# Kernel tuning notes

Measured on AMD Instinct MI355X. Metric: run time of the kernel, lower is better.

Reference implementation:

```python
import jax, jax.numpy as jnp
import numpy as np
from jax.scipy.special import logsumexp

# Model config: alphabet='ACGTZY', collapse='ACGTCA' -> 4 canonical bases, 2 mods
NBASE = 4
NTRANS = 2 * NBASE * (NBASE + 1)          # 40 flip-flop transition states
CAN_NMODS = np.array([1, 1, 0, 0])        # mods per canonical base (A:Y, C:Z)
SIZE = NTRANS + 1 + int(CAN_NMODS.sum())  # 43 linear outputs
LARGE_LOG_VAL = np.float32(50000.0)
T, N, INSIZE = 2000, 128, 256


def _can_indices():
    """Per-canonical-base index groups into the mod block of the linear output."""
    idx, cur = [], 0
    for nm in CAN_NMODS:
        idx.append(np.concatenate([[0], np.arange(cur + 1, cur + 1 + nm)]))
        cur += nm
    return idx

CAN_INDICES = _can_indices()


def setup_inputs() -> dict:
    key = jax.random.key(0)
    k1, k2, k3 = jax.random.split(key, 3)
    x = jax.random.normal(k1, (T, N, INSIZE), dtype=jnp.float32)
    W = jax.random.normal(k2, (SIZE, INSIZE), dtype=jnp.float32) / np.float32(INSIZE ** 0.5)
    b = jax.random.normal(k3, (SIZE,), dtype=jnp.float32) * 0.1
    return {"x": x, "W": W, "b": b}


def global_norm_flipflop(scores):
    """Log-partition of the flip-flop CRF via a sequential log-space scan.

    scores: (T, N, 2*nbase*(nbase+1)).
    """
    Tn, Nn, _ = scores.shape
    # initial state: flip states uniform, flop states ~ -inf
    fwd0 = jnp.concatenate(
        [jnp.zeros((Nn, NBASE), scores.dtype),
         jnp.full((Nn, NBASE), -LARGE_LOG_VAL, scores.dtype)], axis=1)
    logZ0 = logsumexp(fwd0, axis=1, keepdims=True)
    fwd0 = fwd0 - logZ0

    def step(carry, scores_t):
        fwd, logZ = carry
        # (N, nbase+1, 2*nbase): dest-state x source-state transition scores
        curr = fwd[:, None, :] + scores_t.reshape(Nn, NBASE + 1, 2 * NBASE)
        base1 = logsumexp(curr[:, :NBASE], axis=2)                    # to-flip states
        base2 = jnp.logaddexp(curr[:, NBASE, :NBASE],
                              curr[:, NBASE, NBASE:])                 # to-flop (stay)
        new = jnp.concatenate([base1, base2], axis=1)                 # (N, 2*nbase)
        fac = logsumexp(new, axis=1, keepdims=True)
        return (new - fac, logZ + fac), None

    (_, logZ), _ = jax.lax.scan(step, (fwd0, logZ0), scores)
    return scores - logZ / np.float32(Tn)


def reference(x, W, b):
    # Linear projection: (T, N, insize) -> (T, N, size)
    y = jnp.einsum('tnf,cf->tnc', x, W) + b
    # Globally-normalized flip-flop transition scores
    trans = global_norm_flipflop(y[:, :, :NTRANS])
    # Per-canonical-base categorical (can + its mods) log-softmax scores
    mods = [jax.nn.log_softmax(y[:, :, NTRANS + idx], axis=2) for idx in CAN_INDICES]
    return jnp.concatenate([trans] + mods, axis=2)
```

## Files before the change

kernel.cpp:

```cpp
#include <hip/hip_runtime.h>

#define T_DIM 2000
#define N_DIM 128
#define IN_DIM 256
#define OUT_C 46
#define NROWS (T_DIM * N_DIM)
#define NCHUNK 250
#define CLEN 8
#define NSUPER 25
#define SLEN 10

typedef short bf16x8 __attribute__((ext_vector_type(8)));
typedef float f32x4 __attribute__((ext_vector_type(4)));

union F8U { bf16x8 v; uint32_t u[4]; };

__device__ __forceinline__ uint32_t cvtpk(float lo, float hi) {
  uint32_t r;
  asm("v_cvt_pk_bf16_f32 %0, %1, %2" : "=v"(r) : "v"(lo), "v"(hi));
  return r;
}

__device__ __forceinline__ float bf2f(unsigned short u) {
  uint32_t w = (uint32_t)u << 16;
  return __builtin_bit_cast(float, w);
}

#define LDSK 264

__global__ __launch_bounds__(512, 2) void k1_gemm(const float* __restrict__ x,
                                                  const float* __restrict__ W,
                                                  const float* __restrict__ b,
                                                  unsigned short* __restrict__ wsYT,
                                                  float* __restrict__ wsMod) {
  __shared__ unsigned short Wl[43 * LDSK];
  const int tid  = threadIdx.x;
  const int lane = tid & 63;
  const int wv   = tid >> 6;
  const int ln   = lane & 15;
  const int lh   = lane >> 4;

  {
    uint32_t* Wd = reinterpret_cast<uint32_t*>(Wl);
#pragma unroll
    for (int it = 0; it < 11; ++it) {
      int e = tid + it * 512;
      if (e < 43 * 128) {
        int n = e >> 7, kp = e & 127;
        float2 w = *reinterpret_cast<const float2*>(W + (size_t)n * IN_DIM + 2 * kp);
        Wd[n * (LDSK / 2) + kp] = cvtpk(w.x, w.y);
      }
    }
  }
  float bias[3];
#pragma unroll
  for (int nt = 0; nt < 3; ++nt) {
    int n = nt * 16 + ln;
    bias[nt] = b[n > 42 ? 42 : n];
  }
  __syncthreads();

  const int rowbase = blockIdx.x * 512 + wv * 64;
  const float* xbase = x + (size_t)(rowbase + ln) * IN_DIM + lh * 8;

  f32x4 bufA[8], bufB[8];
  f32x4 zero = {0.f, 0.f, 0.f, 0.f};
  f32x4 acc[3] = {zero, zero, zero};

#define LOADH(BUF, T, HF) do {                                               \
    const float* _p = xbase + (size_t)(T) * (16 * IN_DIM) + (HF) * 128;      \
    _Pragma("unroll")                                                        \
    for (int _s = 0; _s < 4; ++_s) {                                         \
      BUF[_s]     = *reinterpret_cast<const f32x4*>(_p + _s * 32);           \
      BUF[_s + 4] = *reinterpret_cast<const f32x4*>(_p + _s * 32 + 4);       \
    }                                                                        \
  } while (0)

#define COMPH(BUF, HF) do {                                                  \
    _Pragma("unroll")                                                        \
    for (int _s2 = 0; _s2 < 4; ++_s2) {                                      \
      F8U _af;                                                               \
      _af.u[0] = cvtpk(BUF[_s2].x, BUF[_s2].y);                              \
      _af.u[1] = cvtpk(BUF[_s2].z, BUF[_s2].w);                              \
      _af.u[2] = cvtpk(BUF[_s2 + 4].x, BUF[_s2 + 4].y);                      \
      _af.u[3] = cvtpk(BUF[_s2 + 4].z, BUF[_s2 + 4].w);                      \
      const int _s = (HF) * 4 + _s2;                                         \
      _Pragma("unroll")                                                      \
      for (int _nt = 0; _nt < 3; ++_nt) {                                    \
        const bf16x8 _bf = *reinterpret_cast<const bf16x8*>(                 \
            &Wl[(_nt * 16 + ln) * LDSK + _s * 32 + lh * 8]);                 \
        acc[_nt] = __builtin_amdgcn_mfma_f32_16x16x32_bf16(_af.v, _bf,       \
                                                           acc[_nt], 0, 0, 0);\
      }                                                                      \
    }                                                                        \
  } while (0)

  LOADH(bufA, 0, 0);
  LOADH(bufB, 0, 1);
#pragma unroll 1
  for (int t = 0; t < 4; ++t) {
    COMPH(bufA, 0);
    if (t < 3) LOADH(bufA, t + 1, 0);
    COMPH(bufB, 1);
    if (t < 3) LOADH(bufB, t + 1, 1);
    const int R0 = rowbase + t * 16;
    const int tt = R0 >> 7;
    const int n0 = (R0 & 127) + lh * 4;
#pragma unroll
    for (int nt = 0; nt < 3; ++nt) {
      const int c = nt * 16 + ln;
      if (nt < 2 || ln < 8) {
        uint32_t d0 = cvtpk(acc[nt][0] + bias[nt], acc[nt][1] + bias[nt]);
        uint32_t d1 = cvtpk(acc[nt][2] + bias[nt], acc[nt][3] + bias[nt]);
        uint2 v; v.x = d0; v.y = d1;
        *reinterpret_cast<uint2*>(wsYT + ((size_t)tt * 40 + c) * 128 + n0) = v;
      } else if (ln < 11) {
        float4 v;
        v.x = acc[2][0] + bias[2]; v.y = acc[2][1] + bias[2];
        v.z = acc[2][2] + bias[2]; v.w = acc[2][3] + bias[2];
        *reinterpret_cast<float4*>(
            wsMod + ((size_t)tt * 3 + (ln - 8)) * 128 + n0) = v;
      }
      acc[nt] = zero;
    }
  }
#undef LOADH
#undef COMPH
}

__global__ __launch_bounds__(128, 1) void k2a_chunk(const unsigned short* __restrict__ wsYT,
                                                    float* __restrict__ wsM,
                                                    float* __restrict__ wsScale) {
  const int c  = blockIdx.x;
  const int n  = threadIdx.x;
  const int t0 = c * CLEN;

  float M[8][8];
  float lsc = 0.f;
  float bufA[40], bufB[40];

#define LOADROW(BUF, TROW) do {                                              \
    const unsigned short* _yr = wsYT + (size_t)(TROW) * (40 * 128) + n;      \
    _Pragma("unroll")                                                        \
    for (int _q = 0; _q < 40; ++_q) BUF[_q] = bf2f(_yr[_q * 128]);           \
  } while (0)

#define INITM(BUF) do {                                                      \
    float _e[40];                                                            \
    _Pragma("unroll")                                                        \
    for (int _q = 0; _q < 40; ++_q) _e[_q] = __expf(BUF[_q]);                \
    _Pragma("unroll")                                                        \
    for (int _i = 0; _i < 4; ++_i)                                           \
      _Pragma("unroll")                                                      \
      for (int _j = 0; _j < 8; ++_j) M[_i][_j] = _e[8*_i+_j];                \
    _Pragma("unroll")                                                        \
    for (int _d = 0; _d < 4; ++_d) {                                         \
      _Pragma("unroll")                                                      \
      for (int _j = 0; _j < 8; ++_j) M[4+_d][_j] = 0.f;                      \
      M[4+_d][_d]   = _e[32+_d];                                             \
      M[4+_d][4+_d] = _e[36+_d];                                             \
    }                                                                        \
  } while (0)

#define STEPM(BUF) do {                                                      \
    float _e[40];                                                            \
    _Pragma("unroll")                                                        \
    for (int _q = 0; _q < 40; ++_q) _e[_q] = __expf(BUF[_q]);                \
    float _nm[8][8];                                                         \
    _Pragma("unroll")                                                        \
    for (int _j = 0; _j < 8; ++_j) {                                         \
      _Pragma("unroll")                                                      \
      for (int _i = 0; _i < 4; ++_i) {                                       \
        float _a = _e[8*_i+0]*M[0][_j] + _e[8*_i+1]*M[1][_j];                \
        float _b = _e[8*_i+2]*M[2][_j] + _e[8*_i+3]*M[3][_j];                \
        float _c = _e[8*_i+4]*M[4][_j] + _e[8*_i+5]*M[5][_j];                \
        float _d = _e[8*_i+6]*M[6][_j] + _e[8*_i+7]*M[7][_j];                \
        _nm[_i][_j] = (_a + _b) + (_c + _d);                                 \
      }                                                                      \
      _Pragma("unroll")                                                      \
      for (int _d2 = 0; _d2 < 4; ++_d2)                                      \
        _nm[4+_d2][_j] = _e[32+_d2]*M[_d2][_j] + _e[36+_d2]*M[4+_d2][_j];    \
    }                                                                        \
    _Pragma("unroll")                                                        \
    for (int _i = 0; _i < 8; ++_i)                                           \
      _Pragma("unroll")                                                      \
      for (int _j = 0; _j < 8; ++_j) M[_i][_j] = _nm[_i][_j];                \
  } while (0)

#define RENORM do {                                                          \
    float _S = 0.f;                                                          \
    _Pragma("unroll")                                                        \
    for (int _i = 0; _i < 8; ++_i)                                           \
      _Pragma("unroll")                                                      \
      for (int _j = 0; _j < 8; ++_j) _S += M[_i][_j];                        \
    lsc += __logf(_S);                                                       \
    const float _inv = 1.0f / _S;                                            \
    _Pragma("unroll")                                                        \
    for (int _i = 0; _i < 8; ++_i)                                           \
      _Pragma("unroll")                                                      \
      for (int _j = 0; _j < 8; ++_j) M[_i][_j] *= _inv;                      \
  } while (0)

  LOADROW(bufA, t0);
  LOADROW(bufB, t0 + 1);
  INITM(bufA);
  LOADROW(bufA, t0 + 2);
  STEPM(bufB);
  LOADROW(bufB, t0 + 3);
  STEPM(bufA);
  LOADROW(bufA, t0 + 4);
  STEPM(bufB);
  RENORM;
  LOADROW(bufB, t0 + 5);
  STEPM(bufA);
  LOADROW(bufA, t0 + 6);
  STEPM(bufB);
  LOADROW(bufB, t0 + 7);
  STEPM(bufA);
  STEPM(bufB);
  RENORM;

#undef LOADROW
#undef INITM
#undef STEPM
#undef RENORM

  float* dst = wsM + (size_t)(c * N_DIM + n) * 64;
#pragma unroll
  for (int q = 0; q < 16; ++q) {
    float4 v;
    v.x = M[q >> 1][(q & 1) * 4 + 0];
    v.y = M[q >> 1][(q & 1) * 4 + 1];
    v.z = M[q >> 1][(q & 1) * 4 + 2];
    v.w = M[q >> 1][(q & 1) * 4 + 3];
    reinterpret_cast<float4*>(dst)[q] = v;
  }
  wsScale[c * N_DIM + n] = lsc;
}

__global__ __launch_bounds__(128, 1) void k2c_super(const float* __restrict__ wsM,
                                                    const float* __restrict__ wsScale,
                                                    float* __restrict__ wsM2,
                                                    float* __restrict__ wsScale2) {
  const int sI = blockIdx.x;
  const int n  = threadIdx.x;
  const int c0 = sI * SLEN;

  float A[8][8], B0[8][8], B1[8][8];
  float lsc = 0.f;
#pragma unroll
  for (int u = 0; u < SLEN; ++u) lsc += wsScale[(c0 + u) * N_DIM + n];

#define LOADM(DST, CIDX) do {                                                \
    const float4* _p = reinterpret_cast<const float4*>(                      \
        wsM + (size_t)((CIDX) * N_DIM + n) * 64);                            \
    _Pragma("unroll")                                                        \
    for (int _q = 0; _q < 16; ++_q) {                                        \
      float4 _v = _p[_q];                                                    \
      DST[_q >> 1][(_q & 1) * 4 + 0] = _v.x;                                 \
      DST[_q >> 1][(_q & 1) * 4 + 1] = _v.y;                                 \
      DST[_q >> 1][(_q & 1) * 4 + 2] = _v.z;                                 \
      DST[_q >> 1][(_q & 1) * 4 + 3] = _v.w;                                 \
    }                                                                        \
  } while (0)

#define FOLD(BB) do {                                                        \
    float C[8][8];                                                           \
    _Pragma("unroll")                                                        \
    for (int _i = 0; _i < 8; ++_i)                                           \
      _Pragma("unroll")                                                      \
      for (int _j = 0; _j < 8; ++_j) {                                       \
        float _a = BB[_i][0]*A[0][_j] + BB[_i][1]*A[1][_j];                  \
        float _b = BB[_i][2]*A[2][_j] + BB[_i][3]*A[3][_j];                  \
        float _c = BB[_i][4]*A[4][_j] + BB[_i][5]*A[5][_j];                  \
        float _d = BB[_i][6]*A[6][_j] + BB[_i][7]*A[7][_j];                  \
        C[_i][_j] = (_a + _b) + (_c + _d);                                   \
      }                                                                      \
    float _S = 0.f;                                                          \
    _Pragma("unroll")                                                        \
    for (int _i = 0; _i < 8; ++_i)                                           \
      _Pragma("unroll")                                                      \
      for (int _j = 0; _j < 8; ++_j) _S += C[_i][_j];                        \
    lsc += __logf(_S);                                                       \
    const float _inv = 1.0f / _S;                                            \
    _Pragma("unroll")                                                        \
    for (int _i = 0; _i < 8; ++_i)                                           \
      _Pragma("unroll")                                                      \
      for (int _j = 0; _j < 8; ++_j) A[_i][_j] = C[_i][_j] * _inv;           \
  } while (0)

  LOADM(A, c0);
  LOADM(B0, c0 + 1);
  LOADM(B1, c0 + 2);
  FOLD(B0); LOADM(B0, c0 + 3);
  FOLD(B1); LOADM(B1, c0 + 4);
  FOLD(B0); LOADM(B0, c0 + 5);
  FOLD(B1); LOADM(B1, c0 + 6);
  FOLD(B0); LOADM(B0, c0 + 7);
  FOLD(B1); LOADM(B1, c0 + 8);
  FOLD(B0); LOADM(B0, c0 + 9);
  FOLD(B1);
  FOLD(B0);
#undef LOADM
#undef FOLD

  float* dst = wsM2 + (size_t)(sI * N_DIM + n) * 64;
#pragma unroll
  for (int q = 0; q < 16; ++q) {
    float4 v;
    v.x = A[q >> 1][(q & 1) * 4 + 0];
    v.y = A[q >> 1][(q & 1) * 4 + 1];
    v.z = A[q >> 1][(q & 1) * 4 + 2];
    v.w = A[q >> 1][(q & 1) * 4 + 3];
    reinterpret_cast<float4*>(dst)[q] = v;
  }
  wsScale2[sI * N_DIM + n] = lsc;
}

__global__ __launch_bounds__(128, 1) void k2b_fold(const float* __restrict__ wsM2,
                                                   const float* __restrict__ wsScale2,
                                                   float* __restrict__ wsLZ) {
  const int tid = threadIdx.x;
  const int n = blockIdx.x * 16 + (tid >> 3);
  const int i = tid & 7;
  const int gbase = (tid & 63) & ~7;

  float4 r0[NSUPER], r1[NSUPER];
  float sc[NSUPER];
#pragma unroll
  for (int s = 0; s < NSUPER; ++s) {
    const float* Mp = wsM2 + ((size_t)(s * N_DIM + n) * 64 + i * 8);
    r0[s] = *reinterpret_cast<const float4*>(Mp);
    r1[s] = *reinterpret_cast<const float4*>(Mp + 4);
    sc[s] = wsScale2[s * N_DIM + n];
  }

  float p[8] = {1.f, 1.f, 1.f, 1.f, 0.f, 0.f, 0.f, 0.f};
  float lz = 0.f;
#pragma unroll
  for (int s = 0; s < NSUPER; ++s) {
    float np = r0[s].x * p[0] + r0[s].y * p[1] + r0[s].z * p[2] + r0[s].w * p[3]
             + r1[s].x * p[4] + r1[s].y * p[5] + r1[s].z * p[6] + r1[s].w * p[7];
#pragma unroll
    for (int j = 0; j < 8; ++j) p[j] = __shfl(np, gbase + j, 64);
    float S = ((p[0] + p[1]) + (p[2] + p[3])) + ((p[4] + p[5]) + (p[6] + p[7]));
    lz += __logf(S) + sc[s];
    const float inv = 1.0f / S;
#pragma unroll
    for (int j = 0; j < 8; ++j) p[j] *= inv;
  }
  if (i == 0) wsLZ[n] = lz * (1.0f / (float)T_DIM);
}

__global__ __launch_bounds__(128, 3) void k3_out(const unsigned short* __restrict__ wsYT,
                                                 const float* __restrict__ wsMod,
                                                 const float* __restrict__ wsLZ,
                                                 float* __restrict__ out) {
  __shared__ float L[256 * 47];
  const int tid = threadIdx.x;
  const int tp  = tid >> 6;
  const int np  = tid & 63;
  const int t   = blockIdx.x * 2 + tp;
  const int n0  = np * 2;

  const float2 sub2 = *reinterpret_cast<const float2*>(wsLZ + n0);
  const unsigned short* yr = wsYT + (size_t)t * (40 * 128) + n0;
  float* r0 = &L[(tp * 128 + n0) * 47];
  float* r1 = r0 + 47;
#pragma unroll
  for (int c = 0; c < 40; ++c) {
    uint32_t v = *reinterpret_cast<const uint32_t*>(yr + c * 128);
    r0[c] = bf2f((unsigned short)(v & 0xFFFF)) - sub2.x;
    r1[c] = bf2f((unsigned short)(v >> 16)) - sub2.y;
  }

  const float* mp = wsMod + (size_t)t * (3 * 128) + n0;
  const float2 y40 = *reinterpret_cast<const float2*>(mp);
  const float2 y41 = *reinterpret_cast<const float2*>(mp + 128);
  const float2 y42 = *reinterpret_cast<const float2*>(mp + 256);

#define MODROW(R, A, B, C)  do {                                             \
    const float m01 = fmaxf(A, B);                                           \
    const float l01 = m01 + log1pf(__expf(fminf(A, B) - m01));               \
    const float m02 = fmaxf(A, C);                                           \
    const float l02 = m02 + log1pf(__expf(fminf(A, C) - m02));               \
    R[40] = A - l01; R[41] = B - l01;                                        \
    R[42] = A - l02; R[43] = C - l02;                                        \
    R[44] = 0.f;     R[45] = 0.f;                                            \
  } while (0)
  MODROW(r0, y40.x, y41.x, y42.x);
  MODROW(r1, y40.y, y41.y, y42.y);
#undef MODROW
  __syncthreads();

  const size_t base = (size_t)blockIdx.x * (256 * 46);
#pragma unroll
  for (int j = 0; j < 92; ++j) {
    const int e = j * 128 + tid;
    const int r = e / 46;
    const int c = e - r * 46;
    out[base + e] = L[r * 47 + c];
  }
}

extern "C" void kernel_launch(void* const* d_in, const int* in_sizes, int n_in,
                              void* d_out, int out_size, void* d_ws, size_t ws_size,
                              hipStream_t stream) {
  (void)in_sizes; (void)n_in; (void)out_size; (void)ws_size;
  const float* x = (const float*)d_in[0];
  const float* W = (const float*)d_in[1];
  const float* b = (const float*)d_in[2];
  float* out = (float*)d_out;

  char* wsb = (char*)d_ws;
  unsigned short* wsYT = (unsigned short*)wsb;
  float* wsMod   = (float*)(wsb + (size_t)T_DIM * 40 * 128 * 2);
  float* wsM     = wsMod + (size_t)T_DIM * 3 * N_DIM;
  float* wsScale = wsM + (size_t)NCHUNK * N_DIM * 64;
  float* wsM2    = wsScale + NCHUNK * N_DIM;
  float* wsScale2= wsM2 + (size_t)NSUPER * N_DIM * 64;
  float* wsLZ    = wsScale2 + NSUPER * N_DIM;

  hipLaunchKernelGGL(k1_gemm,   dim3(NROWS / 512), dim3(512), 0, stream,
                     x, W, b, wsYT, wsMod);
  hipLaunchKernelGGL(k2a_chunk, dim3(NCHUNK), dim3(128), 0, stream,
                     wsYT, wsM, wsScale);
  hipLaunchKernelGGL(k2c_super, dim3(NSUPER), dim3(128), 0, stream,
                     wsM, wsScale, wsM2, wsScale2);
  hipLaunchKernelGGL(k2b_fold,  dim3(8), dim3(128), 0, stream,
                     wsM2, wsScale2, wsLZ);
  hipLaunchKernelGGL(k3_out,    dim3(NROWS / 256), dim3(128), 0, stream,
                     wsYT, wsMod, wsLZ, out);
}
```

Before: 118.9 us.

## Fuse GEMM and per-chunk transfer-matrix product into one kernel via LDS

Merges the projection GEMM and the 8-step chunk matrix-product kernel into a single 1024-thread kernel per chunk. The bf16 scores for the chunk are staged in shared memory so the scan stage reads them from LDS rather than global memory, and one kernel launch is removed. In exchange, only 128 of the 1024 threads run the sequential scan tail while the rest sit idle, and the larger block plus LDS use may lower occupancy. The final output writes also switch to nontemporal stores.

```diff
diff --git a/kernel.cpp b/kernel.cpp
--- a/kernel.cpp
+++ b/kernel.cpp
@@ -27,13 +27,17 @@
 }
 
 #define LDSK 264
-
-__global__ __launch_bounds__(512, 2) void k1_gemm(const float* __restrict__ x,
-                                                  const float* __restrict__ W,
-                                                  const float* __restrict__ b,
-                                                  unsigned short* __restrict__ wsYT,
-                                                  float* __restrict__ wsMod) {
+#define YROW 132
+
+__global__ __launch_bounds__(1024, 4) void k1_fused(const float* __restrict__ x,
+                                                    const float* __restrict__ W,
+                                                    const float* __restrict__ b,
+                                                    unsigned short* __restrict__ wsYT,
+                                                    float* __restrict__ wsMod,
+                                                    float* __restrict__ wsM,
+                                                    float* __restrict__ wsScale) {
   __shared__ unsigned short Wl[43 * LDSK];
+  __shared__ unsigned short Yl[8 * 40 * YROW];
   const int tid  = threadIdx.x;
   const int lane = tid & 63;
   const int wv   = tid >> 6;
@@ -43,8 +47,8 @@
   {
     uint32_t* Wd = reinterpret_cast<uint32_t*>(Wl);
 #pragma unroll
-    for (int it = 0; it < 11; ++it) {
-      int e = tid + it * 512;
+    for (int it = 0; it < 6; ++it) {
+      int e = tid + it * 1024;
       if (e < 43 * 128) {
         int n = e >> 7, kp = e & 127;
         float2 w = *reinterpret_cast<const float2*>(W + (size_t)n * IN_DIM + 2 * kp);
@@ -60,8 +64,10 @@
   }
   __syncthreads();
 
-  const int rowbase = blockIdx.x * 512 + wv * 64;
-  const float* xbase = x + (size_t)(rowbase + ln) * IN_DIM + lh * 8;
+  const int tloc  = wv >> 1;
+  const int nhalf = (wv & 1) * 64;
+  const int tg    = blockIdx.x * 8 + tloc;
+  const float* xbase = x + ((size_t)tg * 128 + nhalf + ln) * IN_DIM + lh * 8;
 
   f32x4 bufA[8], bufB[8];
   f32x4 zero = {0.f, 0.f, 0.f, 0.f};
@@ -103,9 +109,7 @@
     if (t < 3) LOADH(bufA, t + 1, 0);
     COMPH(bufB, 1);
     if (t < 3) LOADH(bufB, t + 1, 1);
-    const int R0 = rowbase + t * 16;
-    const int tt = R0 >> 7;
-    const int n0 = (R0 & 127) + lh * 4;
+    const int n0 = nhalf + t * 16 + lh * 4;
 #pragma unroll
     for (int nt = 0; nt < 3; ++nt) {
       const int c = nt * 16 + ln;
@@ -113,78 +117,65 @@
         uint32_t d0 = cvtpk(acc[nt][0] + bias[nt], acc[nt][1] + bias[nt]);
         uint32_t d1 = cvtpk(acc[nt][2] + bias[nt], acc[nt][3] + bias[nt]);
         uint2 v; v.x = d0; v.y = d1;
-        *reinterpret_cast<uint2*>(wsYT + ((size_t)tt * 40 + c) * 128 + n0) = v;
+        *reinterpret_cast<uint2*>(wsYT + ((size_t)tg * 40 + c) * 128 + n0) = v;
+        *reinterpret_cast<uint2*>(&Yl[(tloc * 40 + c) * YROW + n0]) = v;
       } else if (ln < 11) {
         float4 v;
         v.x = acc[2][0] + bias[2]; v.y = acc[2][1] + bias[2];
         v.z = acc[2][2] + bias[2]; v.w = acc[2][3] + bias[2];
         *reinterpret_cast<float4*>(
-            wsMod + ((size_t)tt * 3 + (ln - 8)) * 128 + n0) = v;
+            wsMod + ((size_t)tg * 3 + (ln - 8)) * 128 + n0) = v;
       }
       acc[nt] = zero;
     }
   }
 #undef LOADH
 #undef COMPH
-}
-
-__global__ __launch_bounds__(128, 1) void k2a_chunk(const unsigned short* __restrict__ wsYT,
-                                                    float* __restrict__ wsM,
-                                                    float* __restrict__ wsScale) {
-  const int c  = blockIdx.x;
-  const int n  = threadIdx.x;
-  const int t0 = c * CLEN;
-
-  float M[8][8];
-  float lsc = 0.f;
-  float bufA[40], bufB[40];
-
-#define LOADROW(BUF, TROW) do {                                              \
-    const unsigned short* _yr = wsYT + (size_t)(TROW) * (40 * 128) + n;      \
-    _Pragma("unroll")                                                        \
-    for (int _q = 0; _q < 40; ++_q) BUF[_q] = bf2f(_yr[_q * 128]);           \
-  } while (0)
-
-#define INITM(BUF) do {                                                      \
-    float _e[40];                                                            \
-    _Pragma("unroll")                                                        \
-    for (int _q = 0; _q < 40; ++_q) _e[_q] = __expf(BUF[_q]);                \
-    _Pragma("unroll")                                                        \
-    for (int _i = 0; _i < 4; ++_i)                                           \
-      _Pragma("unroll")                                                      \
-      for (int _j = 0; _j < 8; ++_j) M[_i][_j] = _e[8*_i+_j];                \
-    _Pragma("unroll")                                                        \
-    for (int _d = 0; _d < 4; ++_d) {                                         \
-      _Pragma("unroll")                                                      \
-      for (int _j = 0; _j < 8; ++_j) M[4+_d][_j] = 0.f;                      \
-      M[4+_d][_d]   = _e[32+_d];                                             \
-      M[4+_d][4+_d] = _e[36+_d];                                             \
+
+  __syncthreads();
+
+  if (tid < 128) {
+    const int n = tid;
+    float M[8][8];
+    float lsc = 0.f;
+
+#define YL(T, Q) bf2f(Yl[((T) * 40 + (Q)) * YROW + n])
+
+    {
+#pragma unroll
+      for (int i = 0; i < 4; ++i)
+#pragma unroll
+        for (int j = 0; j < 8; ++j) M[i][j] = __expf(YL(0, 8 * i + j));
+#pragma unroll
+      for (int d = 0; d < 4; ++d) {
+#pragma unroll
+        for (int j = 0; j < 8; ++j) M[4 + d][j] = 0.f;
+        M[4 + d][d]     = __expf(YL(0, 32 + d));
+        M[4 + d][4 + d] = __expf(YL(0, 36 + d));
+      }
+    }
+
+#define STEPM(T) do {                                                        \
+    float e[40];                                                             \
+    _Pragma("unroll")                                                        \
+    for (int _q = 0; _q < 40; ++_q) e[_q] = __expf(YL(T, _q));               \
+    _Pragma("unroll")                                                        \
+    for (int _j = 0; _j < 8; ++_j) {     \
+      float c0 = M[0][_j], c1 = M[1][_j], c2 = M[2][_j], c3 = M[3][_j];      \
+      float c4 = M[4][_j], c5 = M[5][_j], c6 = M[6][_j], c7 = M[7][_j];      \
+      _Pragma("unroll")                                                      \
+      for (int _i = 0; _i < 4; ++_i) {                                       \
+        float _a = e[8*_i+0]*c0 + e[8*_i+1]*c1;                              \
+        float _b2 = e[8*_i+2]*c2 + e[8*_i+3]*c3;                             \
+        float _c = e[8*_i+4]*c4 + e[8*_i+5]*c5;                              \
+        float _d = e[8*_i+6]*c6 + e[8*_i+7]*c7;                              \
+        M[_i][_j] = (_a + _b2) + (_c + _d);                                  \
+      }                                                                      \
+      M[4][_j] = e[32]*c0 + e[36]*c4;                                        \
+      M[5][_j] = e[33]*c1 + e[37]*c5;                                        \
+      M[6][_j] = e[34]*c2 + e[38]*c6;                                        \
+      M[7][_j] = e[35]*c3 + e[39]*c7;                                        \
     }                                                                        \
-  } while (0)
-
-#define STEPM(BUF) do {                                                      \
-    float _e[40];                                                            \
-    _Pragma("unroll")                                                        \
-    for (int _q = 0; _q < 40; ++_q) _e[_q] = __expf(BUF[_q]);                \
-    float _nm[8][8];                                                         \
-    _Pragma("unroll")                                                        \
-    for (int _j = 0; _j < 8; ++_j) {                                         \
-      _Pragma("unroll")                                                      \
-      for (int _i = 0; _i < 4; ++_i) {                                       \
-        float _a = _e[8*_i+0]*M[0][_j] + _e[8*_i+1]*M[1][_j];                \
-        float _b = _e[8*_i+2]*M[2][_j] + _e[8*_i+3]*M[3][_j];                \
-        float _c = _e[8*_i+4]*M[4][_j] + _e[8*_i+5]*M[5][_j];                \
-        float _d = _e[8*_i+6]*M[6][_j] + _e[8*_i+7]*M[7][_j];                \
-        _nm[_i][_j] = (_a + _b) + (_c + _d);                                 \
-      }                                                                      \
-      _Pragma("unroll")                                                      \
-      for (int _d2 = 0; _d2 < 4; ++_d2)                                      \
-        _nm[4+_d2][_j] = _e[32+_d2]*M[_d2][_j] + _e[36+_d2]*M[4+_d2][_j];    \
-    }                                                                        \
-    _Pragma("unroll")                                                        \
-    for (int _i = 0; _i < 8; ++_i)                                           \
-      _Pragma("unroll")                                                      \
-      for (int _j = 0; _j < 8; ++_j) M[_i][_j] = _nm[_i][_j];                \
   } while (0)
 
 #define RENORM do {                                                          \
@@ -201,41 +192,31 @@
       for (int _j = 0; _j < 8; ++_j) M[_i][_j] *= _inv;                      \
   } while (0)
 
-  LOADROW(bufA, t0);
-  LOADROW(bufB, t0 + 1);
-  INITM(bufA);
-  LOADROW(bufA, t0 + 2);
-  STEPM(bufB);
-  LOADROW(bufB, t0 + 3);
-  STEPM(bufA);
-  LOADROW(bufA, t0 + 4);
-  STEPM(bufB);
-  RENORM;
-  LOADROW(bufB, t0 + 5);
-  STEPM(bufA);
-  LOADROW(bufA, t0 + 6);
-  STEPM(bufB);
-  LOADROW(bufB, t0 + 7);
-  STEPM(bufA);
-  STEPM(bufB);
-  RENORM;
-
-#undef LOADROW
-#undef INITM
+    STEPM(1);
+    STEPM(2);
+    STEPM(3);
+    RENORM;
+    STEPM(4);
+    STEPM(5);
+    STEPM(6);
+    STEPM(7);
+    RENORM;
 #undef STEPM
 #undef RENORM
-
-  float* dst = wsM + (size_t)(c * N_DIM + n) * 64;
-#pragma unroll
-  for (int q = 0; q < 16; ++q) {
-    float4 v;
-    v.x = M[q >> 1][(q & 1) * 4 + 0];
-    v.y = M[q >> 1][(q & 1) * 4 + 1];
-    v.z = M[q >> 1][(q & 1) * 4 + 2];
-    v.w = M[q >> 1][(q & 1) * 4 + 3];
-    reinterpret_cast<float4*>(dst)[q] = v;
-  }
-  wsScale[c * N_DIM + n] = lsc;
+#undef YL
+
+    float* dst = wsM + (size_t)(blockIdx.x * N_DIM + n) * 64;
+#pragma unroll
+    for (int q = 0; q < 16; ++q) {
+      float4 v;
+      v.x = M[q >> 1][(q & 1) * 4 + 0];
+      v.y = M[q >> 1][(q & 1) * 4 + 1];
+      v.z = M[q >> 1][(q & 1) * 4 + 2];
+      v.w = M[q >> 1][(q & 1) * 4 + 3];
+      reinterpret_cast<float4*>(dst)[q] = v;
+    }
+    wsScale[blockIdx.x * N_DIM + n] = lsc;
+  }
 }
 
 __global__ __launch_bounds__(128, 1) void k2c_super(const float* __restrict__ wsM,
@@ -399,7 +380,7 @@
     const int e = j * 128 + tid;
     const int r = e / 46;
     const int c = e - r * 46;
-    out[base + e] = L[r * 47 + c];
+    __builtin_nontemporal_store(L[r * 47 + c], &out[base + e]);
   }
 }
 
@@ -421,10 +402,8 @@
   float* wsScale2= wsM2 + (size_t)NSUPER * N_DIM * 64;
   float* wsLZ    = wsScale2 + NSUPER * N_DIM;
 
-  hipLaunchKernelGGL(k1_gemm,   dim3(NROWS / 512), dim3(512), 0, stream,
-                     x, W, b, wsYT, wsMod);
-  hipLaunchKernelGGL(k2a_chunk, dim3(NCHUNK), dim3(128), 0, stream,
-                     wsYT, wsM, wsScale);
+  hipLaunchKernelGGL(k1_fused,  dim3(NCHUNK), dim3(1024), 0, stream,
+                     x, W, b, wsYT, wsMod, wsM, wsScale);
   hipLaunchKernelGGL(k2c_super, dim3(NSUPER), dim3(128), 0, stream,
                      wsM, wsScale, wsM2, wsScale2);
   hipLaunchKernelGGL(k2b_fold,  dim3(8), dim3(128), 0, stream,
```

New measurement: 131.7 us. 1.11x slower.
